# Kernel optimization log

Hardware: AMD Instinct MI355X
Metric: run time of the kernel (lower is better)

The kernel has to match this reference:

```python
import jax, jax.numpy as jnp
import numpy as np


def _qrnn_forward(X, W, b):
    seq_len, batch, d = X.shape
    H = W.shape[0] // 3
    Y = jnp.einsum('sbd,hd->sbh', X, W) + b  # [S,B,3H]
    Z, F, O = jnp.split(Y, 3, axis=2)
    Z = jnp.tanh(Z)
    F = jax.nn.sigmoid(F)

    # ForgetMult with hidden_init=None: h_0 = f_0*z_0; h_t = f_t*z_t + (1-f_t)*h_{t-1}
    # Equivalent to scan from h_{-1} = 0.
    def step(h_prev, fz):
        f_t, z_t = fz
        h = f_t * z_t + (1.0 - f_t) * h_prev
        return h, h

    h0 = jnp.zeros((batch, H), dtype=X.dtype)
    _, C = jax.lax.scan(step, h0, (F, Z))  # [S,B,H]
    Hout = jax.nn.sigmoid(O) * C
    return Hout, C[-1:, :, :]


def setup_inputs() -> dict:
    key = jax.random.key(0)
    k1, k2, k3 = jax.random.split(key, 3)
    S, B, D, Hdim = 1024, 16, 1024, 1024
    X = jax.random.normal(k1, (S, B, D), dtype=jnp.float32)
    W = jax.random.normal(k2, (3 * Hdim, D), dtype=jnp.float32) * (1.0 / np.sqrt(D))
    b = jax.random.normal(k3, (3 * Hdim,), dtype=jnp.float32) * 0.01
    return {"X": X, "W": W, "b": b}


def reference(X, W, b):
    return _qrnn_forward(X, W, b)
```

## Files before the change

### kernel.cpp

```cpp
#include <hip/hip_runtime.h>
#include <hip/hip_bf16.h>
#include <stdint.h>

typedef __bf16 bf16x8 __attribute__((ext_vector_type(8)));
typedef float f32x4 __attribute__((ext_vector_type(4)));

constexpr int S = 1024, Bsz = 16, Hd = 1024;
constexpr int M = S * Bsz;
constexpr int N = 3 * Hd;
constexpr int K = 1024;
constexpr int BM = 128, BN = 128, BK = 32;
constexpr int NCH = 32, CS = S / NCH;
constexpr int BH = Bsz * Hd;

__device__ __forceinline__ float fast_sigmoid(float x) { return 1.0f / (1.0f + __expf(-x)); }
__device__ __forceinline__ float fast_tanh(float x) { return 2.0f / (1.0f + __expf(-2.0f * x)) - 1.0f; }

__device__ __forceinline__ void gld_lds16(const __bf16* g, __bf16* l) {
  __builtin_amdgcn_global_load_lds(
      (const __attribute__((address_space(1))) void*)g,
      (__attribute__((address_space(3))) void*)l,
      16, 0, 0);
}

__global__ void convert_f32_bf16(const float* __restrict__ src, __bf16* __restrict__ dst, int n8) {
  int i = blockIdx.x * blockDim.x + threadIdx.x;
  if (i >= n8) return;
  const float4* s4 = (const float4*)src;
  float4 a = s4[2 * i], b = s4[2 * i + 1];
  bf16x8 v;
  v[0] = (__bf16)a.x; v[1] = (__bf16)a.y; v[2] = (__bf16)a.z; v[3] = (__bf16)a.w;
  v[4] = (__bf16)b.x; v[5] = (__bf16)b.y; v[6] = (__bf16)b.z; v[7] = (__bf16)b.w;
  *((bf16x8*)dst + i) = v;
}

__global__ __launch_bounds__(256) void gemm_act(const __bf16* __restrict__ A,
                                                const __bf16* __restrict__ Bw,
                                                const float* __restrict__ bias,
                                                __bf16* __restrict__ Y) {
  __shared__ __align__(16) __bf16 As[BM * BK];
  __shared__ __align__(16) __bf16 Bs[BN * BK];
  const int t = threadIdx.x;
  const int lane = t & 63;
  const int wave = t >> 6;
  const int wm = wave >> 1, wn = wave & 1;
  const int tn = blockIdx.x % (N / BN);
  const int tm = blockIdx.x / (N / BN);
  const int m0 = tm * BM, n0 = tn * BN;
  const int lrow = lane & 15;
  const int quad = lane >> 4;

  const int srow = t >> 2;
  const int scw = t & 3;
  const __bf16* gA0 = A + (size_t)(m0 + srow) * K + scw * 8;
  const __bf16* gA1 = gA0 + (size_t)64 * K;
  const __bf16* gB0 = Bw + (size_t)(n0 + srow) * K + scw * 8;
  const __bf16* gB1 = gB0 + (size_t)64 * K;
  __bf16* lA0 = As + wave * 512;
  __bf16* lA1 = As + 2048 + wave * 512;
  __bf16* lB0 = Bs + wave * 512;
  __bf16* lB1 = Bs + 2048 + wave * 512;

  f32x4 acc[4][4] = {};

  for (int k0 = 0; k0 < K; k0 += BK) {
    __syncthreads();
    gld_lds16(gA0, lA0);
    gld_lds16(gA1, lA1);
    gld_lds16(gB0, lB0);
    gld_lds16(gB1, lB1);
    gA0 += BK; gA1 += BK; gB0 += BK; gB1 += BK;
    __syncthreads();

    bf16x8 af[4], bfr[4];
#pragma unroll
    for (int mi = 0; mi < 4; ++mi)
      af[mi] = *(const bf16x8*)(&As[(wm * 64 + mi * 16 + lrow) * BK + quad * 8]);
#pragma unroll
    for (int ni = 0; ni < 4; ++ni)
      bfr[ni] = *(const bf16x8*)(&Bs[(wn * 64 + ni * 16 + lrow) * BK + quad * 8]);
#pragma unroll
    for (int mi = 0; mi < 4; ++mi)
#pragma unroll
      for (int ni = 0; ni < 4; ++ni)
        acc[mi][ni] = __builtin_amdgcn_mfma_f32_16x16x32_bf16(af[mi], bfr[ni], acc[mi][ni], 0, 0, 0);
  }

#pragma unroll
  for (int ni = 0; ni < 4; ++ni) {
    int col = n0 + wn * 64 + ni * 16 + lrow;
    float bv = bias[col];
    bool is_tanh = (col < Hd);
#pragma unroll
    for (int mi = 0; mi < 4; ++mi) {
#pragma unroll
      for (int r = 0; r < 4; ++r) {
        int m = m0 + wm * 64 + mi * 16 + quad * 4 + r;
        float y = acc[mi][ni][r] + bv;
        float v = is_tanh ? fast_tanh(y) : fast_sigmoid(y);
        Y[(size_t)m * N + col] = (__bf16)v;
      }
    }
  }
}

__global__ __launch_bounds__(256) void scan_pass1(const __bf16* __restrict__ Y,
                                                  float* __restrict__ Ac,
                                                  float* __restrict__ Bc) {
  int tid = blockIdx.x * 256 + threadIdx.x;
  int c = tid >> 14;
  int bh = tid & (BH - 1);
  int b = bh >> 10, h = bh & (Hd - 1);
  const size_t sstep = (size_t)Bsz * N;
  size_t base0 = (size_t)b * N + h + (size_t)(c * CS) * sstep;
  float A = 1.0f, B = 0.0f;
  for (int j0 = 0; j0 < CS; j0 += 8) {
    float z[8], f[8];
#pragma unroll
    for (int j = 0; j < 8; ++j) {
      size_t base = base0 + (size_t)(j0 + j) * sstep;
      z[j] = (float)Y[base];
      f[j] = (float)Y[base + Hd];
    }
#pragma unroll
    for (int j = 0; j < 8; ++j) {
      float a = 1.0f - f[j];
      B = fmaf(a, B, f[j] * z[j]);
      A *= a;
    }
  }
  Ac[tid] = A;
  Bc[tid] = B;
}

__global__ __launch_bounds__(256) void scan_pass2(const float* __restrict__ Ac,
                                                  const float* __restrict__ Bc,
                                                  float* __restrict__ hin,
                                                  float* __restrict__ clast) {
  int bh = blockIdx.x * 256 + threadIdx.x;
  float h = 0.0f;
#pragma unroll 4
  for (int c = 0; c < NCH; ++c) {
    hin[c * BH + bh] = h;
    h = fmaf(Ac[c * BH + bh], h, Bc[c * BH + bh]);
  }
  clast[bh] = h;
}

__global__ __launch_bounds__(256) void scan_pass3(const __bf16* __restrict__ Y,
                                                  const float* __restrict__ hin,
                                                  float* __restrict__ hout) {
  int tid = blockIdx.x * 256 + threadIdx.x;
  int c = tid >> 14;
  int bh = tid & (BH - 1);
  int b = bh >> 10, h = bh & (Hd - 1);
  const size_t sstep = (size_t)Bsz * N;
  size_t base0 = (size_t)b * N + h + (size_t)(c * CS) * sstep;
  size_t obase = (size_t)b * Hd + h + (size_t)(c * CS) * BH;
  float hp = hin[tid];
  for (int j0 = 0; j0 < CS; j0 += 8) {
    float z[8], f[8], o[8];
#pragma unroll
    for (int j = 0; j < 8; ++j) {
      size_t base = base0 + (size_t)(j0 + j) * sstep;
      z[j] = (float)Y[base];
      f[j] = (float)Y[base + Hd];
      o[j] = (float)Y[base + 2 * Hd];
    }
#pragma unroll
    for (int j = 0; j < 8; ++j) {
      hp = fmaf(f[j], z[j] - hp, hp);
      hout[obase + (size_t)(j0 + j) * BH] = o[j] * hp;
    }
  }
}

extern "C" void kernel_launch(void* const* d_in, const int* in_sizes, int n_in,
                              void* d_out, int out_size, void* d_ws, size_t ws_size,
                              hipStream_t stream) {
  const float* X = (const float*)d_in[0];
  const float* W = (const float*)d_in[1];
  const float* bias = (const float*)d_in[2];
  float* out = (float*)d_out;

  char* ws = (char*)d_ws;
  __bf16* Xb = (__bf16*)ws;
  __bf16* Wb = (__bf16*)(ws + 33554432);
  __bf16* Yv = (__bf16*)(ws + 39845888);
  float* Ac = (float*)(ws + 39845888 + 100663296);
  float* Bc = Ac + NCH * BH;
  float* hin = Bc + NCH * BH;

  convert_f32_bf16<<<8192, 256, 0, stream>>>(X, Xb, 2097152);
  convert_f32_bf16<<<1536, 256, 0, stream>>>(W, Wb, 393216);

  dim3 ggrid((M / BM) * (N / BN));
  dim3 sgrid(NCH * BH / 256);
  gemm_act<<<ggrid, 256, 0, stream>>>(Xb, Wb, bias, Yv);
  scan_pass1<<<sgrid, 256, 0, stream>>>(Yv, Ac, Bc);
  scan_pass2<<<BH / 256, 256, 0, stream>>>(Ac, Bc, hin, out + 16777216);
  scan_pass3<<<sgrid, 256, 0, stream>>>(Yv, hin, out);
}
```

Measured before the change: 308.9 us.

## Vectorize scan passes to 8 hidden units per thread and merge convert launches

The two scan passes now have each thread handle 8 consecutive hidden units, reading them as bf16x8 vectors and writing outputs as float4 pairs instead of one scalar per thread. This is meant to cut the number of small scalar memory transactions and improve bandwidth use. The two f32-to-bf16 conversion launches are also merged into a single kernel to save one launch. Each scan pass now runs with one eighth as many threads, which lowers parallelism and the latency hiding it provides.

Result: no change. 309.0 us (+0.1%).

```diff
diff --git a/kernel.cpp b/kernel.cpp
--- a/kernel.cpp
+++ b/kernel.cpp
@@ -12,6 +12,8 @@
 constexpr int BM = 128, BN = 128, BK = 32;
 constexpr int NCH = 32, CS = S / NCH;
 constexpr int BH = Bsz * Hd;
+constexpr int NX8 = 2097152;
+constexpr int NW8 = 393216;
 
 __device__ __forceinline__ float fast_sigmoid(float x) { return 1.0f / (1.0f + __expf(-x)); }
 __device__ __forceinline__ float fast_tanh(float x) { return 2.0f / (1.0f + __expf(-2.0f * x)) - 1.0f; }
@@ -23,15 +25,21 @@
       16, 0, 0);
 }
 
-__global__ void convert_f32_bf16(const float* __restrict__ src, __bf16* __restrict__ dst, int n8) {
-  int i = blockIdx.x * blockDim.x + threadIdx.x;
-  if (i >= n8) return;
-  const float4* s4 = (const float4*)src;
-  float4 a = s4[2 * i], b = s4[2 * i + 1];
+__global__ void convert_all(const float* __restrict__ X, const float* __restrict__ W,
+                            __bf16* __restrict__ Xb, __bf16* __restrict__ Wb) {
+  int i = blockIdx.x * 256 + threadIdx.x;
+  const float* s;
+  __bf16* d;
+  int idx;
+  if (i < NX8) { s = X; d = Xb; idx = i; }
+  else if (i < NX8 + NW8) { s = W; d = Wb; idx = i - NX8; }
+  else return;
+  const float4* s4 = (const float4*)s;
+  float4 a = s4[2 * idx], b = s4[2 * idx + 1];
   bf16x8 v;
   v[0] = (__bf16)a.x; v[1] = (__bf16)a.y; v[2] = (__bf16)a.z; v[3] = (__bf16)a.w;
   v[4] = (__bf16)b.x; v[5] = (__bf16)b.y; v[6] = (__bf16)b.z; v[7] = (__bf16)b.w;
-  *((bf16x8*)dst + i) = v;
+  *((bf16x8*)d + idx) = v;
 }
 
 __global__ __launch_bounds__(256) void gemm_act(const __bf16* __restrict__ A,
@@ -108,29 +116,35 @@
                                                   float* __restrict__ Ac,
                                                   float* __restrict__ Bc) {
   int tid = blockIdx.x * 256 + threadIdx.x;
-  int c = tid >> 14;
-  int bh = tid & (BH - 1);
-  int b = bh >> 10, h = bh & (Hd - 1);
+  int c = tid >> 11;
+  int bh8 = tid & 2047;
+  int b = bh8 >> 7, h0 = (bh8 & 127) * 8;
   const size_t sstep = (size_t)Bsz * N;
-  size_t base0 = (size_t)b * N + h + (size_t)(c * CS) * sstep;
-  float A = 1.0f, B = 0.0f;
+  const __bf16* base = Y + (size_t)(c * CS) * sstep + (size_t)b * N + h0;
+  float A[8], Bv[8];
+#pragma unroll
+  for (int l = 0; l < 8; ++l) { A[l] = 1.0f; Bv[l] = 0.0f; }
   for (int j0 = 0; j0 < CS; j0 += 8) {
-    float z[8], f[8];
+    bf16x8 z[8], f[8];
 #pragma unroll
     for (int j = 0; j < 8; ++j) {
-      size_t base = base0 + (size_t)(j0 + j) * sstep;
-      z[j] = (float)Y[base];
-      f[j] = (float)Y[base + Hd];
-    }
-#pragma unroll
-    for (int j = 0; j < 8; ++j) {
-      float a = 1.0f - f[j];
-      B = fmaf(a, B, f[j] * z[j]);
-      A *= a;
-    }
-  }
-  Ac[tid] = A;
-  Bc[tid] = B;
+      const __bf16* p = base + (size_t)(j0 + j) * sstep;
+      z[j] = *(const bf16x8*)p;
+      f[j] = *(const bf16x8*)(p + Hd);
+    }
+#pragma unroll
+    for (int j = 0; j < 8; ++j)
+#pragma unroll
+      for (int l = 0; l < 8; ++l) {
+        float ff = (float)f[j][l];
+        float a = 1.0f - ff;
+        Bv[l] = fmaf(a, Bv[l], ff * (float)z[j][l]);
+        A[l] *= a;
+      }
+  }
+  int ob = c * BH + b * Hd + h0;
+#pragma unroll
+  for (int l = 0; l < 8; ++l) { Ac[ob + l] = A[l]; Bc[ob + l] = Bv[l]; }
 }
 
 __global__ __launch_bounds__(256) void scan_pass2(const float* __restrict__ Ac,
@@ -151,26 +165,37 @@
                                                   const float* __restrict__ hin,
                                                   float* __restrict__ hout) {
   int tid = blockIdx.x * 256 + threadIdx.x;
-  int c = tid >> 14;
-  int bh = tid & (BH - 1);
-  int b = bh >> 10, h = bh & (Hd - 1);
+  int c = tid >> 11;
+  int bh8 = tid & 2047;
+  int b = bh8 >> 7, h0 = (bh8 & 127) * 8;
   const size_t sstep = (size_t)Bsz * N;
-  size_t base0 = (size_t)b * N + h + (size_t)(c * CS) * sstep;
-  size_t obase = (size_t)b * Hd + h + (size_t)(c * CS) * BH;
-  float hp = hin[tid];
-  for (int j0 = 0; j0 < CS; j0 += 8) {
-    float z[8], f[8], o[8];
-#pragma unroll
-    for (int j = 0; j < 8; ++j) {
-      size_t base = base0 + (size_t)(j0 + j) * sstep;
-      z[j] = (float)Y[base];
-      f[j] = (float)Y[base + Hd];
-      o[j] = (float)Y[base + 2 * Hd];
-    }
-#pragma unroll
-    for (int j = 0; j < 8; ++j) {
-      hp = fmaf(f[j], z[j] - hp, hp);
-      hout[obase + (size_t)(j0 + j) * BH] = o[j] * hp;
+  const __bf16* base = Y + (size_t)(c * CS) * sstep + (size_t)b * N + h0;
+  float* ob = hout + (size_t)(c * CS) * BH + (size_t)b * Hd + h0;
+  float hp[8];
+  int hb = c * BH + b * Hd + h0;
+#pragma unroll
+  for (int l = 0; l < 8; ++l) hp[l] = hin[hb + l];
+  for (int j0 = 0; j0 < CS; j0 += 4) {
+    bf16x8 z[4], f[4], o[4];
+#pragma unroll
+    for (int j = 0; j < 4; ++j) {
+      const __bf16* p = base + (size_t)(j0 + j) * sstep;
+      z[j] = *(const bf16x8*)p;
+      f[j] = *(const bf16x8*)(p + Hd);
+      o[j] = *(const bf16x8*)(p + 2 * Hd);
+    }
+#pragma unroll
+    for (int j = 0; j < 4; ++j) {
+      float out8[8];
+#pragma unroll
+      for (int l = 0; l < 8; ++l) {
+        float ff = (float)f[j][l];
+        hp[l] = fmaf(ff, (float)z[j][l] - hp[l], hp[l]);
+        out8[l] = (float)o[j][l] * hp[l];
+      }
+      float* op = ob + (size_t)(j0 + j) * BH;
+      *(float4*)op = make_float4(out8[0], out8[1], out8[2], out8[3]);
+      *(float4*)(op + 4) = make_float4(out8[4], out8[5], out8[6], out8[7]);
     }
   }
 }
@@ -191,11 +216,10 @@
   float* Bc = Ac + NCH * BH;
   float* hin = Bc + NCH * BH;
 
-  convert_f32_bf16<<<8192, 256, 0, stream>>>(X, Xb, 2097152);
-  convert_f32_bf16<<<1536, 256, 0, stream>>>(W, Wb, 393216);
+  convert_all<<<(NX8 + NW8) / 256, 256, 0, stream>>>(X, W, Xb, Wb);
 
   dim3 ggrid((M / BM) * (N / BN));
-  dim3 sgrid(NCH * BH / 256);
+  dim3 sgrid(NCH * BH / 8 / 256);
   gemm_act<<<ggrid, 256, 0, stream>>>(Xb, Wb, bias, Yv);
   scan_pass1<<<sgrid, 256, 0, stream>>>(Yv, Ac, Bc);
   scan_pass2<<<BH / 256, 256, 0, stream>>>(Ac, Bc, hin, out + 16777216);
```
